# Performance work log

Measured on AMD Instinct MI355X. Metric: run time of the kernel, lower is better.

The kernel has to match this reference:

```python
import jax, jax.numpy as jnp
import numpy as np

E = 1024      # h_dim
H = 16        # num_heads
D = E // H    # head_dim = 64
O = 1024      # o_dim == q_dim
EPS = 1e-5


def _rotate_half(x):
    d = x.shape[-1]
    x1, x2 = x[..., : d // 2], x[..., d // 2 :]
    return jnp.concatenate([-x2, x1], axis=-1)


def setup_inputs() -> dict:
    key = jax.random.key(0)
    ks = jax.random.split(key, 12)
    B, S = 8, 1024
    s = 0.02
    return {
        "query": jax.random.normal(ks[0], (B, S, O), jnp.float32),
        "key": jax.random.normal(ks[1], (B, S, O), jnp.float32),
        "value": jax.random.normal(ks[2], (B, S, O), jnp.float32),
        "Wq": jax.random.normal(ks[3], (E, O), jnp.float32) * s,
        "Wk": jax.random.normal(ks[4], (E, O), jnp.float32) * s,
        "Wv": jax.random.normal(ks[5], (E, O), jnp.float32) * s,
        "in_proj_w": jax.random.normal(ks[6], (3 * E, E), jnp.float32) * s,
        "out_proj_w": jax.random.normal(ks[7], (E, E), jnp.float32) * s,
        "proj_w": jax.random.normal(ks[8], (O, E), jnp.float32) * s,
        "gamma": jnp.ones((O,), jnp.float32),
        "beta": jnp.zeros((O,), jnp.float32),
    }


def reference(query, key, value, Wq, Wk, Wv, in_proj_w, out_proj_w, proj_w, gamma, beta):
    B, S, _ = query.shape
    # [B,S,*] -> [S,B,*] then bias-free linears
    q = jnp.swapaxes(query, 0, 1) @ Wq.T  # [S,B,E]
    k = jnp.swapaxes(key, 0, 1) @ Wk.T
    v = jnp.swapaxes(value, 0, 1) @ Wv.T

    # RoPE (faithful quirk: positions indexed along the BATCH axis B)
    inv_freq = 1.0 / (10000.0 ** (jnp.arange(0, D, 2, dtype=jnp.float32) / D))
    t = jnp.arange(B, dtype=jnp.float32)
    freqs = t[:, None] * inv_freq[None, :]            # [B, D/2]
    emb = jnp.concatenate([freqs, freqs], axis=-1)    # [B, D]
    cos = jnp.cos(emb)[None, :, None, :]              # [1,B,1,D]
    sin = jnp.sin(emb)[None, :, None, :]

    q4 = q.reshape(S, B, H, D)
    k4 = k.reshape(S, B, H, D)
    q_emb = (q4 * cos + _rotate_half(q4) * sin).reshape(S, B, E)
    k_emb = (k4 * cos + _rotate_half(k4) * sin).reshape(S, B, E)

    # nn.MultiheadAttention (bias=False, batch_first=False)
    Wqa, Wka, Wva = in_proj_w[:E], in_proj_w[E : 2 * E], in_proj_w[2 * E :]
    qp = (q_emb @ Wqa.T).reshape(S, B, H, D)
    kp = (k_emb @ Wka.T).reshape(S, B, H, D)
    vp = (v @ Wva.T).reshape(S, B, H, D)

    scale = 1.0 / np.sqrt(D).astype(np.float32)
    scores = jnp.einsum("sbhd,tbhd->bhst", qp, kp) * scale  # [B,H,S,S]
    attn = jax.nn.softmax(scores, axis=-1)
    o = jnp.einsum("bhst,tbhd->sbhd", attn, vp).reshape(S, B, E)
    o = o @ out_proj_w.T                                     # [S,B,E]

    # output proj + residual + LayerNorm
    ob = jnp.swapaxes(o, 0, 1) @ proj_w.T                    # [B,S,O]
    x = query + ob
    mu = jnp.mean(x, axis=-1, keepdims=True)
    var = jnp.mean((x - mu) ** 2, axis=-1, keepdims=True)
    return (x - mu) * jax.lax.rsqrt(var + EPS) * gamma + beta
```

## Files before the change

kernel.cpp:

```cpp
#include <hip/hip_runtime.h>
#include <hip/hip_bf16.h>
#include <stdint.h>

typedef __bf16 bf16;
typedef __attribute__((ext_vector_type(8))) __bf16 bf16x8;
typedef __attribute__((ext_vector_type(4))) float f32x4;

#define NEG_LN10K_32 (-0.28782313662425575f)

__device__ __forceinline__ bf16x8 cvt8(f32x4 a, f32x4 b) {
    bf16x8 r;
    r[0] = (bf16)a[0]; r[1] = (bf16)a[1]; r[2] = (bf16)a[2]; r[3] = (bf16)a[3];
    r[4] = (bf16)b[0]; r[5] = (bf16)b[1]; r[6] = (bf16)b[2]; r[7] = (bf16)b[3];
    return r;
}

__device__ __forceinline__ void async_copy16(bf16* lds, const bf16* g) {
    __builtin_amdgcn_global_load_lds((const __attribute__((address_space(1))) void*)g,
                                     (__attribute__((address_space(3))) void*)lds, 16, 0, 0);
}

__global__ __launch_bounds__(256) void wconv6(
    const float* __restrict__ s0, const float* __restrict__ s1, const float* __restrict__ s2,
    const float* __restrict__ s3, const float* __restrict__ s4, const float* __restrict__ s5,
    bf16* __restrict__ d0, bf16* __restrict__ d1, bf16* __restrict__ d2,
    bf16* __restrict__ d3, bf16* __restrict__ d4, bf16* __restrict__ d5)
{
    const int z = blockIdx.z;
    const float* src; bf16* dst;
    switch (z) {
        case 0: src = s0; dst = d0; break;
        case 1: src = s1; dst = d1; break;
        case 2: src = s2; dst = d2; break;
        case 3: src = s3; dst = d3; break;
        case 4: src = s4; dst = d4; break;
        default: src = s5; dst = d5; break;
    }
    const size_t i = ((size_t)blockIdx.x * 256 + threadIdx.x) * 8;
    *(bf16x8*)(dst + i) = cvt8(*(const f32x4*)(src + i), *(const f32x4*)(src + i + 4));
}

__global__ __launch_bounds__(256) void prepT(
    const float* __restrict__ in0, const float* __restrict__ in1,
    bf16* __restrict__ out0, bf16* __restrict__ out1)
{
    const float* in = blockIdx.z ? in1 : in0;
    bf16* out       = blockIdx.z ? out1 : out0;
    __shared__ float tile[64 * 65];
    const int t  = threadIdx.x;
    const int i0 = blockIdx.y * 64, j0 = blockIdx.x * 64;
    const int r  = t >> 2, cg = (t & 3) * 16;
#pragma unroll
    for (int c = 0; c < 16; c += 4) {
        const f32x4 v = *(const f32x4*)(in + (size_t)(i0 + r) * 1024 + j0 + cg + c);
        tile[r * 65 + cg + c + 0] = v[0];
        tile[r * 65 + cg + c + 1] = v[1];
        tile[r * 65 + cg + c + 2] = v[2];
        tile[r * 65 + cg + c + 3] = v[3];
    }
    __syncthreads();
    bf16x8 o0v, o1v;
#pragma unroll
    for (int ii = 0; ii < 8; ++ii) {
        o0v[ii] = (bf16)tile[(cg + ii) * 65 + r];
        o1v[ii] = (bf16)tile[(cg + 8 + ii) * 65 + r];
    }
    bf16* dst = out + (size_t)(j0 + r) * 1024 + i0 + cg;
    *(bf16x8*)dst       = o0v;
    *(bf16x8*)(dst + 8) = o1v;
}

template<int AF32, int WF32>
__global__ __launch_bounds__(256) void gemm_bt(
    const void* __restrict__ A0v, const void* __restrict__ A1v, const void* __restrict__ A2v,
    const void* __restrict__ W0v, const void* __restrict__ W1v, const void* __restrict__ W2v,
    bf16* __restrict__ C0, bf16* __restrict__ C1, bf16* __restrict__ C2,
    const float* __restrict__ R0, int rope_mask)
{
    const int z = blockIdx.z;
    const void* Av = (z == 0) ? A0v : ((z == 1) ? A1v : A2v);
    const void* Wp = (z == 0) ? W0v : ((z == 1) ? W1v : W2v);
    bf16*       C  = (z == 0) ? C0 : ((z == 1) ? C1 : C2);
    const float* R = (z == 0) ? R0 : nullptr;
    const bool doRope = ((rope_mask >> z) & 1) != 0;

    __shared__ __attribute__((aligned(16))) bf16 sA[128 * 32];
    __shared__ __attribute__((aligned(16))) bf16 sB[128 * 32];

    const int t    = threadIdx.x;
    const int w    = t >> 6;
    const int lane = t & 63;
    const int l16  = lane & 15;
    const int quad = lane >> 4;
    const int wrow = w >> 1;
    const int wcol = w & 1;

    int m0, n0;
    if (gridDim.y == 64) {
        const int fs   = blockIdx.y * 8 + blockIdx.x;
        const int xcd  = fs & 7;
        const int slot = fs >> 3;
        m0 = ((xcd << 3) | (slot >> 3)) * 128;
        n0 = (slot & 7) * 128;
    } else {
        m0 = blockIdx.y * 128;
        n0 = blockIdx.x * 128;
    }

    const int sgr = ((t & 3) ^ ((t >> 3) & 3)) * 8;
    const size_t aOff = (size_t)(m0 + (t >> 2)) * 1024 + sgr;
    const size_t wOff = (size_t)(n0 + (t >> 2)) * 1024 + sgr;
    const int qs = (quad ^ ((l16 >> 1) & 3)) * 8;

    f32x4 acc[4][4];
#pragma unroll
    for (int i = 0; i < 4; ++i)
#pragma unroll
        for (int j = 0; j < 4; ++j)
            acc[i][j] = (f32x4){0.f, 0.f, 0.f, 0.f};

    for (int k0 = 0; k0 < 1024; k0 += 32) {
        bf16x8 va0, va1, vb0, vb1;
        if (AF32) {
            const float* g = (const float*)Av;
            va0 = cvt8(*(const f32x4*)(g + aOff + k0),             *(const f32x4*)(g + aOff + k0 + 4));
            va1 = cvt8(*(const f32x4*)(g + aOff + 64 * 1024 + k0), *(const f32x4*)(g + aOff + 64 * 1024 + k0 + 4));
        }
        if (WF32) {
            const float* g = (const float*)Wp;
            vb0 = cvt8(*(const f32x4*)(g + wOff + k0),             *(const f32x4*)(g + wOff + k0 + 4));
            vb1 = cvt8(*(const f32x4*)(g + wOff + 64 * 1024 + k0), *(const f32x4*)(g + wOff + 64 * 1024 + k0 + 4));
        }
        __syncthreads();
        if (AF32) {
            *(bf16x8*)&sA[t * 8]        = va0;
            *(bf16x8*)&sA[t * 8 + 2048] = va1;
        } else {
            const bf16* g = (const bf16*)Av;
            async_copy16(sA + w * 512,        g + aOff + k0);
            async_copy16(sA + w * 512 + 2048, g + aOff + 64 * 1024 + k0);
        }
        if (WF32) {
            *(bf16x8*)&sB[t * 8]        = vb0;
            *(bf16x8*)&sB[t * 8 + 2048] = vb1;
        } else {
            const bf16* g = (const bf16*)Wp;
            async_copy16(sB + w * 512,        g + wOff + k0);
            async_copy16(sB + w * 512 + 2048, g + wOff + 64 * 1024 + k0);
        }
        __syncthreads();

        bf16x8 af[4], bw[4];
#pragma unroll
        for (int mi = 0; mi < 4; ++mi)
            af[mi] = *(const bf16x8*)&sA[(wrow * 64 + mi * 16 + l16) * 32 + qs];
#pragma unroll
        for (int ni = 0; ni < 4; ++ni)
            bw[ni] = *(const bf16x8*)&sB[(wcol * 64 + ni * 16 + l16) * 32 + qs];
#pragma unroll
        for (int mi = 0; mi < 4; ++mi)
#pragma unroll
            for (int ni = 0; ni < 4; ++ni)
                acc[mi][ni] = __builtin_amdgcn_mfma_f32_16x16x32_bf16(af[mi], bw[ni], acc[mi][ni], 0, 0, 0);
    }

    if (doRope) {
        const float bb = (float)(m0 >> 10);
        float s0, c0v, s1, c1v;
        sincosf(bb * expf((float)l16 * NEG_LN10K_32), &s0, &c0v);
        sincosf(bb * expf((float)(16 + l16) * NEG_LN10K_32), &s1, &c1v);
#pragma unroll
        for (int mi = 0; mi < 4; ++mi) {
#pragma unroll
            for (int r = 0; r < 4; ++r) {
                float x1 = acc[mi][0][r], x2 = acc[mi][2][r];
                acc[mi][0][r] = x1 * c0v - x2 * s0;
                acc[mi][2][r] = x2 * c0v + x1 * s0;
                x1 = acc[mi][1][r]; x2 = acc[mi][3][r];
                acc[mi][1][r] = x1 * c1v - x2 * s1;
                acc[mi][3][r] = x2 * c1v + x1 * s1;
            }
        }
    }

#pragma unroll
    for (int mi = 0; mi < 4; ++mi) {
#pragma unroll
        for (int ni = 0; ni < 4; ++ni) {
            const int col = n0 + wcol * 64 + ni * 16 + l16;
#pragma unroll
            for (int r = 0; r < 4; ++r) {
                const int row = m0 + wrow * 64 + mi * 16 + quad * 4 + r;
                float v = acc[mi][ni][r];
                if (R) v += R[(size_t)row * 1024 + col];
                C[(size_t)row * 1024 + col] = (bf16)v;
            }
        }
    }
}

__global__ __launch_bounds__(256) void attn_kernel(
    bf16* __restrict__ QP, const bf16* __restrict__ KP, const bf16* __restrict__ VP)
{
    const int fs   = blockIdx.y * 8 + blockIdx.x;
    const int xcd  = fs & 7;
    const int slot = fs >> 3;
    const int qt   = slot & 7;
    const int bh   = (xcd << 4) | (slot >> 3);
    const int tb = (bh >> 4) << 10;
    const int fb = (bh & 15) << 6;

    __shared__ __attribute__((aligned(16))) bf16 sK0[64 * 32];
    __shared__ __attribute__((aligned(16))) bf16 sK1[64 * 32];
    __shared__ __attribute__((aligned(16))) bf16 sVt[64 * 72];
    __shared__ __attribute__((aligned(16))) bf16 sP[4][32 * 72];

    const int t    = threadIdx.x;
    const int w    = t >> 6;
    const int lane = t & 63;
    const int l16  = lane & 15;
    const int quad = lane >> 4;

    const int sgr = ((t & 3) ^ ((t >> 3) & 3)) * 8;
    const int qs  = (quad ^ ((l16 >> 1) & 3)) * 8;

    bf16x8 qf[2][2];
#pragma unroll
    for (int mi = 0; mi < 2; ++mi)
#pragma unroll
        for (int kd = 0; kd < 2; ++kd)
            qf[mi][kd] = *(const bf16x8*)&QP[(size_t)(tb + qt * 128 + w * 32 + mi * 16 + l16) * 1024
                                            + fb + kd * 32 + quad * 8];

    f32x4 oacc[2][4];
#pragma unroll
    for (int i = 0; i < 2; ++i)
#pragma unroll
        for (int j = 0; j < 4; ++j)
            oacc[i][j] = (f32x4){0.f, 0.f, 0.f, 0.f};
    float psum[2][4];
#pragma unroll
    for (int i = 0; i < 2; ++i)
#pragma unroll
        for (int r = 0; r < 4; ++r) psum[i][r] = 0.f;

    for (int kt = 0; kt < 16; ++kt) {
        const bf16* kRow = KP + (size_t)(tb + kt * 64 + (t >> 2)) * 1024 + fb + sgr;
        const bf16x8 vk0 = *(const bf16x8*)(kRow);
        const bf16x8 vk1 = *(const bf16x8*)(kRow + 32);
        const bf16* vRow = VP + (size_t)(tb + kt * 64 + lane) * 1024 + fb;
        const bf16x8 vv0 = *(const bf16x8*)(vRow + w * 8);
        const bf16x8 vv1 = *(const bf16x8*)(vRow + (w + 4) * 8);

        __syncthreads();
        *(bf16x8*)&sK0[t * 8] = vk0;
        *(bf16x8*)&sK1[t * 8] = vk1;
#pragma unroll
        for (int j = 0; j < 8; ++j) sVt[(w * 8 + j) * 72 + lane]       = vv0[j];
#pragma unroll
        for (int j = 0; j < 8; ++j) sVt[((w + 4) * 8 + j) * 72 + lane] = vv1[j];
        __syncthreads();

        bf16x8 kf[4][2];
#pragma unroll
        for (int ni = 0; ni < 4; ++ni) {
            kf[ni][0] = *(const bf16x8*)&sK0[(ni * 16 + l16) * 32 + qs];
            kf[ni][1] = *(const bf16x8*)&sK1[(ni * 16 + l16) * 32 + qs];
        }
        f32x4 sfr[2][4];
#pragma unroll
        for (int mi = 0; mi < 2; ++mi)
#pragma unroll
            for (int ni = 0; ni < 4; ++ni) {
                f32x4 a = (f32x4){0.f, 0.f, 0.f, 0.f};
                a = __builtin_amdgcn_mfma_f32_16x16x32_bf16(qf[mi][0], kf[ni][0], a, 0, 0, 0);
                a = __builtin_amdgcn_mfma_f32_16x16x32_bf16(qf[mi][1], kf[ni][1], a, 0, 0, 0);
                sfr[mi][ni] = a * 0.125f;
            }

#pragma unroll
        for (int mi = 0; mi < 2; ++mi)
#pragma unroll
            for (int ni = 0; ni < 4; ++ni)
#pragma unroll
                for (int r = 0; r < 4; ++r) {
                    const float p = __expf(sfr[mi][ni][r]);
                    sfr[mi][ni][r] = p;
                    psum[mi][r] += p;
                }

        bf16* sPw = &sP[w][0];
#pragma unroll
        for (int mi = 0; mi < 2; ++mi)
#pragma unroll
            for (int ni = 0; ni < 4; ++ni)
#pragma unroll
                for (int r = 0; r < 4; ++r)
                    sPw[(mi * 16 + quad * 4 + r) * 72 + ni * 16 + l16] = (bf16)sfr[mi][ni][r];
        asm volatile("s_waitcnt lgkmcnt(0)" ::: "memory");

#pragma unroll
        for (int kd = 0; kd < 2; ++kd) {
            bf16x8 pf[2], vf[4];
#pragma unroll
            for (int mi = 0; mi < 2; ++mi)
                pf[mi] = *(const bf16x8*)&sPw[(mi * 16 + l16) * 72 + kd * 32 + quad * 8];
#pragma unroll
            for (int di = 0; di < 4; ++di)
                vf[di] = *(const bf16x8*)&sVt[(di * 16 + l16) * 72 + kd * 32 + quad * 8];
#pragma unroll
            for (int mi = 0; mi < 2; ++mi)
#pragma unroll
                for (int di = 0; di < 4; ++di)
                    oacc[mi][di] = __builtin_amdgcn_mfma_f32_16x16x32_bf16(pf[mi], vf[di], oacc[mi][di], 0, 0, 0);
        }
    }

#pragma unroll
    for (int mi = 0; mi < 2; ++mi) {
#pragma unroll
        for (int r = 0; r < 4; ++r) {
            float l = psum[mi][r];
            l += __shfl_xor(l, 1);
            l += __shfl_xor(l, 2);
            l += __shfl_xor(l, 4);
            l += __shfl_xor(l, 8);
            const float inv = 1.f / l;
            const int row = tb + qt * 128 + w * 32 + mi * 16 + quad * 4 + r;
#pragma unroll
            for (int di = 0; di < 4; ++di) {
                const int col = fb + di * 16 + l16;
                QP[(size_t)row * 1024 + col] = (bf16)(oacc[mi][di][r] * inv);
            }
        }
    }
}

__global__ __launch_bounds__(128) void ln_kernel(const bf16* __restrict__ X,
                                                 const float* __restrict__ G,
                                                 const float* __restrict__ Bt,
                                                 float* __restrict__ Y)
{
    const int row = blockIdx.x;
    const int t   = threadIdx.x;
    const size_t base = (size_t)row * 1024 + t * 8;
    const bf16x8 xv = *(const bf16x8*)(X + base);
    float f[8];
    float s = 0.f, s2 = 0.f;
#pragma unroll
    for (int j = 0; j < 8; ++j) { f[j] = (float)xv[j]; s += f[j]; s2 += f[j] * f[j]; }
#pragma unroll
    for (int off = 1; off < 64; off <<= 1) { s += __shfl_xor(s, off); s2 += __shfl_xor(s2, off); }
    __shared__ float ss[2], ssq[2];
    if ((t & 63) == 0) { ss[t >> 6] = s; ssq[t >> 6] = s2; }
    __syncthreads();
    s  = ss[0] + ss[1];
    s2 = ssq[0] + ssq[1];
    const float mu  = s * (1.f / 1024.f);
    const float inv = rsqrtf(s2 * (1.f / 1024.f) - mu * mu + 1e-5f);
    const f32x4 g0 = *(const f32x4*)(G + t * 8);
    const f32x4 g1 = *(const f32x4*)(G + t * 8 + 4);
    const f32x4 b0 = *(const f32x4*)(Bt + t * 8);
    const f32x4 b1 = *(const f32x4*)(Bt + t * 8 + 4);
    f32x4 y0, y1;
#pragma unroll
    for (int j = 0; j < 4; ++j) {
        y0[j] = (f[j]     - mu) * inv * g0[j] + b0[j];
        y1[j] = (f[j + 4] - mu) * inv * g1[j] + b1[j];
    }
    *(f32x4*)(Y + base)     = y0;
    *(f32x4*)(Y + base + 4) = y1;
}

extern "C" void kernel_launch(void* const* d_in, const int* in_sizes, int n_in,
                              void* d_out, int out_size, void* d_ws, size_t ws_size,
                              hipStream_t stream)
{
    const float* query = (const float*)d_in[0];
    const float* key   = (const float*)d_in[1];
    const float* value = (const float*)d_in[2];
    const float* Wq    = (const float*)d_in[3];
    const float* Wk    = (const float*)d_in[4];
    const float* Wv    = (const float*)d_in[5];
    const float* ipw   = (const float*)d_in[6];
    const float* opw   = (const float*)d_in[7];
    const float* pw    = (const float*)d_in[8];
    const float* gamma = (const float*)d_in[9];
    const float* beta  = (const float*)d_in[10];

    const size_t ACT = (size_t)8192 * 1024;
    const size_t MW  = 1048576;
    bf16* o0 = (bf16*)d_out;
    bf16* o1 = o0 + ACT;

    dim3 blk(256);
    dim3 g3(8, 64, 3);
    dim3 g1(8, 64, 1);
    dim3 ga(8, 128);

    const bool full = ws_size >= (6 * MW + 2 * ACT) * sizeof(bf16);

    if (full) {
        bf16* wq  = (bf16*)d_ws;
        bf16* wk  = wq + MW;
        bf16* wqa = wq + 2 * MW;
        bf16* wka = wq + 3 * MW;
        bf16* Fv  = wq + 4 * MW;
        bf16* Fo  = wq + 5 * MW;
        bf16* sltA = wq + 6 * MW;
        bf16* sltB = sltA + ACT;
        bf16* tWva = sltA;
        bf16* tpw  = sltA + MW;
        bf16* WvT  = sltB;
        bf16* opwT = sltB + MW;

        wconv6<<<dim3(512, 1, 6), blk, 0, stream>>>(
            Wq, Wk, ipw, ipw + MW, ipw + 2 * MW, pw,
            wq, wk, wqa, wka, tWva, tpw);
        prepT<<<dim3(16, 16, 2), blk, 0, stream>>>(Wv, opw, WvT, opwT);
        gemm_bt<0, 0><<<dim3(8, 8, 2), blk, 0, stream>>>(
            tWva, tpw, tpw, WvT, opwT, opwT, Fv, Fo, Fo, nullptr, 0);
        gemm_bt<1, 0><<<g3, blk, 0, stream>>>(query, key, value, wq, wk, Fv,
                                              sltA, sltB, o0, nullptr, 0b011);
        gemm_bt<0, 0><<<g1, blk, 0, stream>>>(sltA, sltA, sltA, wqa, wqa, wqa,
                                              o1, o1, o1, nullptr, 0);
        gemm_bt<0, 0><<<g1, blk, 0, stream>>>(sltB, sltB, sltB, wka, wka, wka,
                                              sltA, sltA, sltA, nullptr, 0);
        attn_kernel<<<ga, blk, 0, stream>>>(o1, sltA, o0);
        gemm_bt<0, 0><<<g1, blk, 0, stream>>>(o1, o1, o1, Fo, Fo, Fo,
                                              sltB, sltB, sltB, query, 0);
        ln_kernel<<<8192, 128, 0, stream>>>(sltB, gamma, beta, (float*)d_out);
    } else {
        bf16* b0 = (bf16*)d_ws;
        bf16* b1 = b0 + ACT;
        gemm_bt<1, 1><<<g3, blk, 0, stream>>>(query, key, value, Wq, Wk, Wv,
                                              b0, b1, o0, nullptr, 0b011);
        gemm_bt<0, 1><<<g1, blk, 0, stream>>>(o0, o0, o0, ipw + 2 * MW, ipw, ipw,
                                              o1, o1, o1, nullptr, 0);
        gemm_bt<0, 1><<<g1, blk, 0, stream>>>(b0, b0, b0, ipw, ipw, ipw,
                                              o0, o0, o0, nullptr, 0);
        gemm_bt<0, 1><<<g1, blk, 0, stream>>>(b1, b1, b1, ipw + MW, ipw, ipw,
                                              b0, b0, b0, nullptr, 0);
        attn_kernel<<<ga, blk, 0, stream>>>(o0, b0, o1);
        gemm_bt<0, 1><<<g1, blk, 0, stream>>>(o0, o0, o0, opw, opw, opw,
                                              b0, b0, b0, nullptr, 0);
        gemm_bt<0, 1><<<g1, blk, 0, stream>>>(b0, b0, b0, pw, pw, pw,
                                              b1, b1, b1, query, 0);
        ln_kernel<<<8192, 128, 0, stream>>>(b1, gamma, beta, (float*)d_out);
    }
}
```

Before: 454.1 us.

## Double-buffer GEMM shared tiles and prefetch K/V tiles in attention

The projection GEMM now uses two shared-memory buffers per operand. It issues global loads (async LDS copies for bf16 inputs, register prefetch for fp32 inputs) for the next K-slice while MFMAs run on the current one, with hand-placed waitcnt and barrier instructions replacing the paired __syncthreads. The attention kernel prefetches the next K/V tile into registers before the compute of the current tile. This hides global memory latency but doubles LDS usage in the GEMM and raises register pressure, which may lower occupancy; the hand-written vmcnt counts also risk correctness if the compiler reorders loads.

```diff
diff --git a/kernel.cpp b/kernel.cpp
--- a/kernel.cpp
+++ b/kernel.cpp
@@ -84,8 +84,8 @@
     const float* R = (z == 0) ? R0 : nullptr;
     const bool doRope = ((rope_mask >> z) & 1) != 0;
 
-    __shared__ __attribute__((aligned(16))) bf16 sA[128 * 32];
-    __shared__ __attribute__((aligned(16))) bf16 sB[128 * 32];
+    __shared__ __attribute__((aligned(16))) bf16 sA[2][128 * 32];
+    __shared__ __attribute__((aligned(16))) bf16 sB[2][128 * 32];
 
     const int t    = threadIdx.x;
     const int w    = t >> 6;
@@ -112,6 +112,41 @@
     const size_t wOff = (size_t)(n0 + (t >> 2)) * 1024 + sgr;
     const int qs = (quad ^ ((l16 >> 1) & 3)) * 8;
 
+    f32x4 arg[4], brg[4];
+
+    auto loadAreg = [&](int k0) {
+        const float* g = (const float*)Av;
+        arg[0] = *(const f32x4*)(g + aOff + k0);
+        arg[1] = *(const f32x4*)(g + aOff + k0 + 4);
+        arg[2] = *(const f32x4*)(g + aOff + 65536 + k0);
+        arg[3] = *(const f32x4*)(g + aOff + 65536 + k0 + 4);
+    };
+    auto loadBreg = [&](int k0) {
+        const float* g = (const float*)Wp;
+        brg[0] = *(const f32x4*)(g + wOff + k0);
+        brg[1] = *(const f32x4*)(g + wOff + k0 + 4);
+        brg[2] = *(const f32x4*)(g + wOff + 65536 + k0);
+        brg[3] = *(const f32x4*)(g + wOff + 65536 + k0 + 4);
+    };
+    auto writeAreg = [&](int b) {
+        *(bf16x8*)&sA[b][t * 8]        = cvt8(arg[0], arg[1]);
+        *(bf16x8*)&sA[b][t * 8 + 2048] = cvt8(arg[2], arg[3]);
+    };
+    auto writeBreg = [&](int b) {
+        *(bf16x8*)&sB[b][t * 8]        = cvt8(brg[0], brg[1]);
+        *(bf16x8*)&sB[b][t * 8 + 2048] = cvt8(brg[2], brg[3]);
+    };
+    auto stageAasync = [&](int k0, int b) {
+        const bf16* g = (const bf16*)Av;
+        async_copy16(&sA[b][w * 512],        g + aOff + k0);
+        async_copy16(&sA[b][w * 512 + 2048], g + aOff + 65536 + k0);
+    };
+    auto stageBasync = [&](int k0, int b) {
+        const bf16* g = (const bf16*)Wp;
+        async_copy16(&sB[b][w * 512],        g + wOff + k0);
+        async_copy16(&sB[b][w * 512 + 2048], g + wOff + 65536 + k0);
+    };
+
     f32x4 acc[4][4];
 #pragma unroll
     for (int i = 0; i < 4; ++i)
@@ -119,49 +154,66 @@
         for (int j = 0; j < 4; ++j)
             acc[i][j] = (f32x4){0.f, 0.f, 0.f, 0.f};
 
+    if constexpr (AF32) loadAreg(0);
+    if constexpr (WF32) loadBreg(0);
+    if constexpr (!AF32) stageAasync(0, 0);
+    if constexpr (!WF32) stageBasync(0, 0);
+    if constexpr (AF32 && WF32)      asm volatile("s_waitcnt vmcnt(0)" ::: "memory");
+    else if constexpr (AF32 || WF32) asm volatile("s_waitcnt vmcnt(2)" ::: "memory");
+    if constexpr (AF32) writeAreg(0);
+    if constexpr (WF32) writeBreg(0);
+    if constexpr (AF32) loadAreg(32);
+    if constexpr (WF32) loadBreg(32);
+    if constexpr (!AF32 && !WF32)    asm volatile("s_waitcnt vmcnt(0) lgkmcnt(0)\ns_barrier" ::: "memory");
+    else if constexpr (AF32 && WF32) asm volatile("s_waitcnt lgkmcnt(0)\ns_barrier" ::: "memory");
+    else                             asm volatile("s_waitcnt vmcnt(4) lgkmcnt(0)\ns_barrier" ::: "memory");
+
     for (int k0 = 0; k0 < 1024; k0 += 32) {
-        bf16x8 va0, va1, vb0, vb1;
-        if (AF32) {
-            const float* g = (const float*)Av;
-            va0 = cvt8(*(const f32x4*)(g + aOff + k0),             *(const f32x4*)(g + aOff + k0 + 4));
-            va1 = cvt8(*(const f32x4*)(g + aOff + 64 * 1024 + k0), *(const f32x4*)(g + aOff + 64 * 1024 + k0 + 4));
-        }
-        if (WF32) {
-            const float* g = (const float*)Wp;
-            vb0 = cvt8(*(const f32x4*)(g + wOff + k0),             *(const f32x4*)(g + wOff + k0 + 4));
-            vb1 = cvt8(*(const f32x4*)(g + wOff + 64 * 1024 + k0), *(const f32x4*)(g + wOff + 64 * 1024 + k0 + 4));
-        }
-        __syncthreads();
-        if (AF32) {
-            *(bf16x8*)&sA[t * 8]        = va0;
-            *(bf16x8*)&sA[t * 8 + 2048] = va1;
-        } else {
-            const bf16* g = (const bf16*)Av;
-            async_copy16(sA + w * 512,        g + aOff + k0);
-            async_copy16(sA + w * 512 + 2048, g + aOff + 64 * 1024 + k0);
-        }
-        if (WF32) {
-            *(bf16x8*)&sB[t * 8]        = vb0;
-            *(bf16x8*)&sB[t * 8 + 2048] = vb1;
-        } else {
-            const bf16* g = (const bf16*)Wp;
-            async_copy16(sB + w * 512,        g + wOff + k0);
-            async_copy16(sB + w * 512 + 2048, g + wOff + 64 * 1024 + k0);
-        }
-        __syncthreads();
+        const int buf = (k0 >> 5) & 1;
+        const int nb  = buf ^ 1;
+        const int nxt = k0 + 32;
+
+        if (nxt < 1024) {
+            if constexpr (!AF32) stageAasync(nxt, nb);
+            if constexpr (!WF32) stageBasync(nxt, nb);
+        }
 
         bf16x8 af[4], bw[4];
 #pragma unroll
         for (int mi = 0; mi < 4; ++mi)
-            af[mi] = *(const bf16x8*)&sA[(wrow * 64 + mi * 16 + l16) * 32 + qs];
+            af[mi] = *(const bf16x8*)&sA[buf][(wrow * 64 + mi * 16 + l16) * 32 + qs];
 #pragma unroll
         for (int ni = 0; ni < 4; ++ni)
-            bw[ni] = *(const bf16x8*)&sB[(wcol * 64 + ni * 16 + l16) * 32 + qs];
+            bw[ni] = *(const bf16x8*)&sB[buf][(wcol * 64 + ni * 16 + l16) * 32 + qs];
 #pragma unroll
         for (int mi = 0; mi < 4; ++mi)
 #pragma unroll
             for (int ni = 0; ni < 4; ++ni)
                 acc[mi][ni] = __builtin_amdgcn_mfma_f32_16x16x32_bf16(af[mi], bw[ni], acc[mi][ni], 0, 0, 0);
+
+        if constexpr (AF32 || WF32) {
+            if (nxt < 1024) {
+                if constexpr (AF32 && WF32) asm volatile("s_waitcnt vmcnt(0)" ::: "memory");
+                else                        asm volatile("s_waitcnt vmcnt(2)" ::: "memory");
+                if constexpr (AF32) writeAreg(nb);
+                if constexpr (WF32) writeBreg(nb);
+                if (k0 + 64 < 1024) {
+                    if constexpr (AF32) loadAreg(k0 + 64);
+                    if constexpr (WF32) loadBreg(k0 + 64);
+                }
+            }
+        }
+
+        if (nxt < 1024) {
+            if constexpr (!AF32 && !WF32)
+                asm volatile("s_waitcnt vmcnt(0) lgkmcnt(0)\ns_barrier" ::: "memory");
+            else if constexpr (AF32 && WF32)
+                asm volatile("s_waitcnt lgkmcnt(0)\ns_barrier" ::: "memory");
+            else {
+                if (k0 + 64 < 1024) asm volatile("s_waitcnt vmcnt(4) lgkmcnt(0)\ns_barrier" ::: "memory");
+                else                asm volatile("s_waitcnt vmcnt(0) lgkmcnt(0)\ns_barrier" ::: "memory");
+            }
+        }
     }
 
     if (doRope) {
@@ -244,14 +296,22 @@
 #pragma unroll
         for (int r = 0; r < 4; ++r) psum[i][r] = 0.f;
 
+    auto ldK = [&](int kt, bf16x8& a, bf16x8& b) {
+        const bf16* kRow = KP + (size_t)(tb + kt * 64 + (t >> 2)) * 1024 + fb + sgr;
+        a = *(const bf16x8*)(kRow);
+        b = *(const bf16x8*)(kRow + 32);
+    };
+    auto ldV = [&](int kt, bf16x8& a, bf16x8& b) {
+        const bf16* vRow = VP + (size_t)(tb + kt * 64 + lane) * 1024 + fb;
+        a = *(const bf16x8*)(vRow + w * 8);
+        b = *(const bf16x8*)(vRow + (w + 4) * 8);
+    };
+
+    bf16x8 vk0, vk1, vv0, vv1;
+    ldK(0, vk0, vk1);
+    ldV(0, vv0, vv1);
+
     for (int kt = 0; kt < 16; ++kt) {
-        const bf16* kRow = KP + (size_t)(tb + kt * 64 + (t >> 2)) * 1024 + fb + sgr;
-        const bf16x8 vk0 = *(const bf16x8*)(kRow);
-        const bf16x8 vk1 = *(const bf16x8*)(kRow + 32);
-        const bf16* vRow = VP + (size_t)(tb + kt * 64 + lane) * 1024 + fb;
-        const bf16x8 vv0 = *(const bf16x8*)(vRow + w * 8);
-        const bf16x8 vv1 = *(const bf16x8*)(vRow + (w + 4) * 8);
-
         __syncthreads();
         *(bf16x8*)&sK0[t * 8] = vk0;
         *(bf16x8*)&sK1[t * 8] = vk1;
@@ -259,6 +319,13 @@
         for (int j = 0; j < 8; ++j) sVt[(w * 8 + j) * 72 + lane]       = vv0[j];
 #pragma unroll
         for (int j = 0; j < 8; ++j) sVt[((w + 4) * 8 + j) * 72 + lane] = vv1[j];
+
+        bf16x8 nk0, nk1, nv0, nv1;
+        const bool more = (kt + 1 < 16);
+        if (more) {
+            ldK(kt + 1, nk0, nk1);
+            ldV(kt + 1, nv0, nv1);
+        }
         __syncthreads();
 
         bf16x8 kf[4][2];
@@ -314,6 +381,8 @@
                 for (int di = 0; di < 4; ++di)
                     oacc[mi][di] = __builtin_amdgcn_mfma_f32_16x16x32_bf16(pf[mi], vf[di], oacc[mi][di], 0, 0, 0);
         }
+
+        if (more) { vk0 = nk0; vk1 = nk1; vv0 = nv0; vv1 = nv1; }
     }
 
 #pragma unroll
```

Result: slower. 493.0 us (+8.6%).

## Double GEMM K-tile depth to 64 with new XOR swizzle layout

Applied to the files above, without the earlier changes.

Raises the K step of the projection GEMM from 32 to 64, halving the number of loop iterations and the barrier pairs per tile. Shared-memory staging is re-laid out with a row-wise 8-way XOR swizzle, and each thread now loads four 16-byte chunks for both the fp32-convert path and the async-copy path. This amortizes synchronization and global-load latency over twice the MFMA work, at the cost of double the shared memory and more registers holding fp32 staging data, which may reduce occupancy.

```diff
diff --git a/kernel.cpp b/kernel.cpp
--- a/kernel.cpp
+++ b/kernel.cpp
@@ -84,8 +84,8 @@
     const float* R = (z == 0) ? R0 : nullptr;
     const bool doRope = ((rope_mask >> z) & 1) != 0;
 
-    __shared__ __attribute__((aligned(16))) bf16 sA[128 * 32];
-    __shared__ __attribute__((aligned(16))) bf16 sB[128 * 32];
+    __shared__ __attribute__((aligned(16))) bf16 sA[128 * 64];
+    __shared__ __attribute__((aligned(16))) bf16 sB[128 * 64];
 
     const int t    = threadIdx.x;
     const int w    = t >> 6;
@@ -107,10 +107,56 @@
         n0 = blockIdx.x * 128;
     }
 
-    const int sgr = ((t & 3) ^ ((t >> 3) & 3)) * 8;
-    const size_t aOff = (size_t)(m0 + (t >> 2)) * 1024 + sgr;
-    const size_t wOff = (size_t)(n0 + (t >> 2)) * 1024 + sgr;
-    const int qs = (quad ^ ((l16 >> 1) & 3)) * 8;
+    const int aLane = (int)(lane >> 3) * 1024 + (((lane & 7) ^ (lane >> 3)) << 3);
+    const int qs0 = ((quad    ) ^ (l16 & 7)) * 8;
+    const int qs1 = ((quad + 4) ^ (l16 & 7)) * 8;
+
+    const int rRow = t >> 1;
+    int rCol[4];
+#pragma unroll
+    for (int j = 0; j < 4; ++j)
+        rCol[j] = ((((t & 1) * 4 + j) ^ (rRow & 7)) << 3);
+
+    f32x4 arg[8], brg[8];
+
+    auto loadAreg = [&](int k0) {
+        const float* g = (const float*)Av + (size_t)(m0 + rRow) * 1024 + k0;
+#pragma unroll
+        for (int j = 0; j < 4; ++j) {
+            arg[2 * j]     = *(const f32x4*)(g + rCol[j]);
+            arg[2 * j + 1] = *(const f32x4*)(g + rCol[j] + 4);
+        }
+    };
+    auto writeAreg = [&]() {
+#pragma unroll
+        for (int j = 0; j < 4; ++j)
+            *(bf16x8*)&sA[t * 32 + j * 8] = cvt8(arg[2 * j], arg[2 * j + 1]);
+    };
+    auto loadBreg = [&](int k0) {
+        const float* g = (const float*)Wp + (size_t)(n0 + rRow) * 1024 + k0;
+#pragma unroll
+        for (int j = 0; j < 4; ++j) {
+            brg[2 * j]     = *(const f32x4*)(g + rCol[j]);
+            brg[2 * j + 1] = *(const f32x4*)(g + rCol[j] + 4);
+        }
+    };
+    auto writeBreg = [&]() {
+#pragma unroll
+        for (int j = 0; j < 4; ++j)
+            *(bf16x8*)&sB[t * 32 + j * 8] = cvt8(brg[2 * j], brg[2 * j + 1]);
+    };
+    auto stageAasync = [&](int k0) {
+        const bf16* g = (const bf16*)Av + (size_t)m0 * 1024 + aLane + k0;
+#pragma unroll
+        for (int c = 0; c < 4; ++c)
+            async_copy16(sA + (c * 4 + w) * 512, g + (size_t)(c * 4 + w) * 8 * 1024);
+    };
+    auto stageBasync = [&](int k0) {
+        const bf16* g = (const bf16*)Wp + (size_t)n0 * 1024 + aLane + k0;
+#pragma unroll
+        for (int c = 0; c < 4; ++c)
+            async_copy16(sB + (c * 4 + w) * 512, g + (size_t)(c * 4 + w) * 8 * 1024);
+    };
 
     f32x4 acc[4][4];
 #pragma unroll
@@ -119,49 +165,30 @@
         for (int j = 0; j < 4; ++j)
             acc[i][j] = (f32x4){0.f, 0.f, 0.f, 0.f};
 
-    for (int k0 = 0; k0 < 1024; k0 += 32) {
-        bf16x8 va0, va1, vb0, vb1;
-        if (AF32) {
-            const float* g = (const float*)Av;
-            va0 = cvt8(*(const f32x4*)(g + aOff + k0),             *(const f32x4*)(g + aOff + k0 + 4));
-            va1 = cvt8(*(const f32x4*)(g + aOff + 64 * 1024 + k0), *(const f32x4*)(g + aOff + 64 * 1024 + k0 + 4));
-        }
-        if (WF32) {
-            const float* g = (const float*)Wp;
-            vb0 = cvt8(*(const f32x4*)(g + wOff + k0),             *(const f32x4*)(g + wOff + k0 + 4));
-            vb1 = cvt8(*(const f32x4*)(g + wOff + 64 * 1024 + k0), *(const f32x4*)(g + wOff + 64 * 1024 + k0 + 4));
-        }
+    for (int k0 = 0; k0 < 1024; k0 += 64) {
+        if (AF32) loadAreg(k0);
+        if (WF32) loadBreg(k0);
         __syncthreads();
-        if (AF32) {
-            *(bf16x8*)&sA[t * 8]        = va0;
-            *(bf16x8*)&sA[t * 8 + 2048] = va1;
-        } else {
-            const bf16* g = (const bf16*)Av;
-            async_copy16(sA + w * 512,        g + aOff + k0);
-            async_copy16(sA + w * 512 + 2048, g + aOff + 64 * 1024 + k0);
-        }
-        if (WF32) {
-            *(bf16x8*)&sB[t * 8]        = vb0;
-            *(bf16x8*)&sB[t * 8 + 2048] = vb1;
-        } else {
-            const bf16* g = (const bf16*)Wp;
-            async_copy16(sB + w * 512,        g + wOff + k0);
-            async_copy16(sB + w * 512 + 2048, g + wOff + 64 * 1024 + k0);
-        }
+        if (AF32) writeAreg(); else stageAasync(k0);
+        if (WF32) writeBreg(); else stageBasync(k0);
         __syncthreads();
 
-        bf16x8 af[4], bw[4];
-#pragma unroll
-        for (int mi = 0; mi < 4; ++mi)
-            af[mi] = *(const bf16x8*)&sA[(wrow * 64 + mi * 16 + l16) * 32 + qs];
-#pragma unroll
-        for (int ni = 0; ni < 4; ++ni)
-            bw[ni] = *(const bf16x8*)&sB[(wcol * 64 + ni * 16 + l16) * 32 + qs];
-#pragma unroll
-        for (int mi = 0; mi < 4; ++mi)
+#pragma unroll
+        for (int kk = 0; kk < 2; ++kk) {
+            const int qs = kk ? qs1 : qs0;
+            bf16x8 af[4], bw[4];
+#pragma unroll
+            for (int mi = 0; mi < 4; ++mi)
+                af[mi] = *(const bf16x8*)&sA[(wrow * 64 + mi * 16 + l16) * 64 + qs];
 #pragma unroll
             for (int ni = 0; ni < 4; ++ni)
-                acc[mi][ni] = __builtin_amdgcn_mfma_f32_16x16x32_bf16(af[mi], bw[ni], acc[mi][ni], 0, 0, 0);
+                bw[ni] = *(const bf16x8*)&sB[(wcol * 64 + ni * 16 + l16) * 64 + qs];
+#pragma unroll
+            for (int mi = 0; mi < 4; ++mi)
+#pragma unroll
+                for (int ni = 0; ni < 4; ++ni)
+                    acc[mi][ni] = __builtin_amdgcn_mfma_f32_16x16x32_bf16(af[mi], bw[ni], acc[mi][ni], 0, 0, 0);
+        }
     }
 
     if (doRope) {
```

After: 444.3 us. -2.2%, faster.
